# Performance work log

Hardware: AMD Instinct MI355X
Metric: run time of the kernel (lower is better)

Reference implementation:

```python
import jax, jax.numpy as jnp
import numpy as np

B, S, D, H = 8, 1024, 768, 12
DH = D // H


def setup_inputs() -> dict:
    key = jax.random.key(0)
    ks = jax.random.split(key, 6)
    scale = 1.0 / np.sqrt(D)
    return {
        "inputs": jax.random.normal(ks[0], (B, S, D), dtype=jnp.float32),
        "Wq": jax.random.normal(ks[1], (D, D), dtype=jnp.float32) * scale,
        "bq": jnp.zeros((D,), jnp.float32),
        "Wk": jax.random.normal(ks[2], (D, D), dtype=jnp.float32) * scale,
        "bk": jnp.zeros((D,), jnp.float32),
        "Wv": jax.random.normal(ks[3], (D, D), dtype=jnp.float32) * scale,
        "bv": jnp.zeros((D,), jnp.float32),
        "Wo": jax.random.normal(ks[4], (D, D), dtype=jnp.float32) * scale,
        "bo": jnp.zeros((D,), jnp.float32),
    }


def _split_heads(x):
    # [B,S,D] -> [B,H,S,DH]
    b, s, _ = x.shape
    return x.reshape(b, s, H, DH).transpose(0, 2, 1, 3)


def reference(inputs, Wq, bq, Wk, bk, Wv, bv, Wo, bo):
    q = _split_heads(inputs @ Wq + bq)
    k = _split_heads(inputs @ Wk + bk)
    v = _split_heads(inputs @ Wv + bv)
    # scaled dot-product attention; scale = sqrt(projection_dim)
    scores = jnp.einsum("bhqd,bhkd->bhqk", q, k) / jnp.sqrt(jnp.float32(DH))
    weights = jax.nn.softmax(scores, axis=-1)
    attn = jnp.einsum("bhqk,bhkd->bhqd", weights, v)
    attn = attn.transpose(0, 2, 1, 3).reshape(inputs.shape[0], -1, D)
    return attn @ Wo + bo
```

## Files before the change

kernel.cpp:

```cpp
#include <hip/hip_runtime.h>
#include <math.h>

#define B 8
#define S 1024
#define D 768
#define H 12
#define DH 64
#define M_TOT (B * S)

#define QSCALE 0.18033688011112042f

typedef short bf16x8 __attribute__((ext_vector_type(8)));
typedef float f32x4 __attribute__((ext_vector_type(4)));
typedef unsigned u32x4 __attribute__((ext_vector_type(4)));

__device__ __forceinline__ unsigned short f2bf(float x) {
    unsigned u = __builtin_bit_cast(unsigned, x);
    u = (u + 0x7FFFu + ((u >> 16) & 1u)) >> 16;
    return (unsigned short)u;
}
__device__ __forceinline__ unsigned short f2bf_ru(float x) {
    return (unsigned short)((__builtin_bit_cast(unsigned, x) + 0x8000u) >> 16);
}
__device__ __forceinline__ unsigned pk2bf_ru(float a, float b) {
    unsigned ua = __builtin_bit_cast(unsigned, a) + 0x8000u;
    unsigned ub = __builtin_bit_cast(unsigned, b) + 0x8000u;
    return __builtin_amdgcn_perm(ub, ua, 0x07060302u);
}

__device__ __forceinline__ void async16(const unsigned short* g, unsigned short* l) {
    __builtin_amdgcn_global_load_lds((const __attribute__((address_space(1))) void*)g,
                                     (__attribute__((address_space(3))) void*)l, 16, 0, 0);
}

__device__ __forceinline__ void stage_tiles(const unsigned short* __restrict__ A,
                                            const unsigned short* __restrict__ Bt,
                                            unsigned short* At, unsigned short* Bs,
                                            int m0, int n0, int k0, int w, int srow, int scol) {
#pragma unroll
    for (int c = 0; c < 2; ++c) {
        const int cc = w * 2 + c;
        const int row = cc * 16 + srow;
        async16(&A[(size_t)(m0 + row) * D + k0 + scol], &At[cc * 512]);
        async16(&Bt[(size_t)(n0 + row) * D + k0 + scol], &Bs[cc * 512]);
    }
}

__global__ __launch_bounds__(256) void prep(const float* __restrict__ inputs,
                                            unsigned short* __restrict__ Abf,
                                            const float* W0, const float* W1,
                                            const float* W2, const float* W3,
                                            unsigned short* T0, unsigned short* T1,
                                            unsigned short* T2, unsigned short* T3) {
    const int bid = blockIdx.x;
    const int t = threadIdx.x;
    if (bid < 6144) {
        const int i = (bid * 256 + t) * 4;
        const float4 v = *(const float4*)&inputs[i];
        ushort4 o;
        o.x = f2bf(v.x); o.y = f2bf(v.y); o.z = f2bf(v.z); o.w = f2bf(v.w);
        *(ushort4*)&Abf[i] = o;
    } else {
        const int id = bid - 6144;
        const int z = id / 144;
        const int rem = id % 144;
        const int kx = rem % 12, ny = rem / 12;
        const float* Wsrc[4] = {W0, W1, W2, W3};
        unsigned short* Tdst[4] = {T0, T1, T2, T3};
        const float* Wm = Wsrc[z];
        unsigned short* Tm = Tdst[z];
        __shared__ float tile[64][65];
        const int r = t >> 4, c4 = (t & 15) * 4;
        const int k0 = kx * 64, n0 = ny * 64;
#pragma unroll
        for (int rr = 0; rr < 4; ++rr) {
            const float4 v = *(const float4*)&Wm[(size_t)(k0 + r + rr * 16) * D + n0 + c4];
            tile[r + rr * 16][c4 + 0] = v.x;
            tile[r + rr * 16][c4 + 1] = v.y;
            tile[r + rr * 16][c4 + 2] = v.z;
            tile[r + rr * 16][c4 + 3] = v.w;
        }
        __syncthreads();
#pragma unroll
        for (int rr = 0; rr < 4; ++rr) {
            const int nr = r + rr * 16;
            ushort4 o;
            o.x = f2bf(tile[c4 + 0][nr]);
            o.y = f2bf(tile[c4 + 1][nr]);
            o.z = f2bf(tile[c4 + 2][nr]);
            o.w = f2bf(tile[c4 + 3][nr]);
            *(ushort4*)&Tm[(size_t)(n0 + nr) * D + k0 + c4] = o;
        }
    }
}

__global__ __launch_bounds__(256) void gemm_qkv(const unsigned short* __restrict__ A,
                                                const unsigned short* __restrict__ Wtq,
                                                const unsigned short* __restrict__ Wtk,
                                                const unsigned short* __restrict__ Wtv,
                                                const float* __restrict__ bq,
                                                const float* __restrict__ bk,
                                                const float* __restrict__ bv,
                                                unsigned short* __restrict__ Qb,
                                                unsigned short* __restrict__ Kb,
                                                unsigned short* __restrict__ Vtb) {
    __shared__ unsigned short At[3][128 * 32];
    __shared__ unsigned short Bs[3][128 * 32];
    const int z = blockIdx.z;
    const unsigned short* Bt = (z == 0) ? Wtq : (z == 1) ? Wtk : Wtv;
    const float* bias = (z == 0) ? bq : (z == 1) ? bk : bv;
    const float scale = (z == 0) ? QSCALE : 1.0f;

    const int t = threadIdx.x;
    const int w = t >> 6, lane = t & 63;
    const int quad = lane >> 4, l15 = lane & 15;
    const int m0 = blockIdx.x * 128, n0 = blockIdx.y * 128;
    const int wm = (w & 1) * 64, wn = (w >> 1) * 64;
    const int srow = lane >> 2, scol = (lane & 3) * 8;
    const int NT = D / 32;

    f32x4 acc[4][4];
#pragma unroll
    for (int i = 0; i < 4; ++i)
#pragma unroll
        for (int j = 0; j < 4; ++j) acc[i][j] = (f32x4){0.f, 0.f, 0.f, 0.f};

    stage_tiles(A, Bt, At[0], Bs[0], m0, n0, 0, w, srow, scol);
    stage_tiles(A, Bt, At[1], Bs[1], m0, n0, 32, w, srow, scol);
    int cur = 0, nxt = 2;
    for (int kt = 0; kt < NT; ++kt) {
        if (kt + 1 < NT) {
            __asm__ volatile("s_waitcnt vmcnt(4)" ::: "memory");
        } else {
            __asm__ volatile("s_waitcnt vmcnt(0)" ::: "memory");
        }
        __asm__ volatile("s_barrier" ::: "memory");
        if (kt + 2 < NT) {
            stage_tiles(A, Bt, At[nxt], Bs[nxt], m0, n0, (kt + 2) * 32, w, srow, scol);
            nxt = (nxt == 2) ? 0 : nxt + 1;
        }
        const unsigned short* Atc = At[cur];
        const unsigned short* Bsc = Bs[cur];
        cur = (cur == 2) ? 0 : cur + 1;
        bf16x8 af[4], bfr[4];
#pragma unroll
        for (int i = 0; i < 4; ++i)
            af[i] = *(const bf16x8*)&Atc[(wm + i * 16 + l15) * 32 + quad * 8];
#pragma unroll
        for (int j = 0; j < 4; ++j)
            bfr[j] = *(const bf16x8*)&Bsc[(wn + j * 16 + l15) * 32 + quad * 8];
#pragma unroll
        for (int i = 0; i < 4; ++i)
#pragma unroll
            for (int j = 0; j < 4; ++j)
                acc[i][j] = __builtin_amdgcn_mfma_f32_16x16x32_bf16(af[i], bfr[j], acc[i][j], 0, 0, 0);
    }

#pragma unroll
    for (int j = 0; j < 4; ++j) {
        const int col = n0 + wn + j * 16 + l15;
        const float bv2 = bias[col];
#pragma unroll
        for (int i = 0; i < 4; ++i) {
            const int row0 = m0 + wm + i * 16 + quad * 4;
            if (z < 2) {
                unsigned short* C = (z == 0) ? Qb : Kb;
#pragma unroll
                for (int r = 0; r < 4; ++r)
                    C[(size_t)(row0 + r) * D + col] = f2bf_ru((acc[i][j][r] + bv2) * scale);
            } else {
                const int h = col >> 6, dh = col & 63;
                const int bb = row0 >> 10, s0 = row0 & 1023;
                const int g = (s0 & 63) >> 2;
                const int kap = ((g >> 3) << 5) | ((g & 3) << 3) | (((g >> 2) & 1) << 2);
                const int s0p = (s0 & ~63) | kap;
                uint2 u;
                u.x = pk2bf_ru(acc[i][j][0] + bv2, acc[i][j][1] + bv2);
                u.y = pk2bf_ru(acc[i][j][2] + bv2, acc[i][j][3] + bv2);
                *(uint2*)&Vtb[((size_t)(bb * H + h) * DH + dh) * S + s0p] = u;
            }
        }
    }
}

__global__ __launch_bounds__(256) void gemm_out(const unsigned short* __restrict__ A,
                                                const unsigned short* __restrict__ Bt,
                                                const float* __restrict__ bias,
                                                float* __restrict__ C) {
    __shared__ unsigned short At[3][128 * 32];
    __shared__ unsigned short Bs[3][128 * 32];
    const int t = threadIdx.x;
    const int w = t >> 6, lane = t & 63;
    const int quad = lane >> 4, l15 = lane & 15;
    const int m0 = blockIdx.x * 128, n0 = blockIdx.y * 128;
    const int wm = (w & 1) * 64, wn = (w >> 1) * 64;
    const int srow = lane >> 2, scol = (lane & 3) * 8;
    const int NT = D / 32;

    f32x4 acc[4][4];
#pragma unroll
    for (int i = 0; i < 4; ++i)
#pragma unroll
        for (int j = 0; j < 4; ++j) acc[i][j] = (f32x4){0.f, 0.f, 0.f, 0.f};

    stage_tiles(A, Bt, At[0], Bs[0], m0, n0, 0, w, srow, scol);
    stage_tiles(A, Bt, At[1], Bs[1], m0, n0, 32, w, srow, scol);
    int cur = 0, nxt = 2;
    for (int kt = 0; kt < NT; ++kt) {
        if (kt + 1 < NT) {
            __asm__ volatile("s_waitcnt vmcnt(4)" ::: "memory");
        } else {
            __asm__ volatile("s_waitcnt vmcnt(0)" ::: "memory");
        }
        __asm__ volatile("s_barrier" ::: "memory");
        if (kt + 2 < NT) {
            stage_tiles(A, Bt, At[nxt], Bs[nxt], m0, n0, (kt + 2) * 32, w, srow, scol);
            nxt = (nxt == 2) ? 0 : nxt + 1;
        }
        const unsigned short* Atc = At[cur];
        const unsigned short* Bsc = Bs[cur];
        cur = (cur == 2) ? 0 : cur + 1;
        bf16x8 af[4], bfr[4];
#pragma unroll
        for (int i = 0; i < 4; ++i)
            af[i] = *(const bf16x8*)&Atc[(wm + i * 16 + l15) * 32 + quad * 8];
#pragma unroll
        for (int j = 0; j < 4; ++j)
            bfr[j] = *(const bf16x8*)&Bsc[(wn + j * 16 + l15) * 32 + quad * 8];
#pragma unroll
        for (int i = 0; i < 4; ++i)
#pragma unroll
            for (int j = 0; j < 4; ++j)
                acc[i][j] = __builtin_amdgcn_mfma_f32_16x16x32_bf16(af[i], bfr[j], acc[i][j], 0, 0, 0);
    }

#pragma unroll
    for (int j = 0; j < 4; ++j) {
        const int col = n0 + wn + j * 16 + l15;
        const float bv = bias[col];
#pragma unroll
        for (int i = 0; i < 4; ++i) {
            const int row0 = m0 + wm + i * 16 + quad * 4;
#pragma unroll
            for (int r = 0; r < 4; ++r) C[(size_t)(row0 + r) * D + col] = acc[i][j][r] + bv;
        }
    }
}

__global__ __launch_bounds__(256) void attn_mfma(const unsigned short* __restrict__ Qg,
                                                 const unsigned short* __restrict__ Kg,
                                                 const unsigned short* __restrict__ Vtg,
                                                 unsigned short* __restrict__ ATT) {
    __shared__ unsigned short Ks[3][2 * 64 * 32];
    __shared__ unsigned short Vs[3][2 * 64 * 32];

    const int t = threadIdx.x;
    const int w = t >> 6, lane = t & 63;
    const int quad = lane >> 4, l15 = lane & 15;
    const int bh = blockIdx.x % (B * H);
    const int q0 = (blockIdx.x / (B * H)) * 128;
    const int b = bh / H, h = bh % H;

    bf16x8 qb[2][2];
#pragma unroll
    for (int qh = 0; qh < 2; ++qh) {
        const size_t qoff = ((size_t)(b * S + q0 + w * 32 + qh * 16 + l15)) * D + h * DH;
        qb[qh][0] = *(const bf16x8*)&Qg[qoff + quad * 8];
        qb[qh][1] = *(const bf16x8*)&Qg[qoff + 32 + quad * 8];
    }

    f32x4 o[2][4];
#pragma unroll
    for (int qh = 0; qh < 2; ++qh)
#pragma unroll
        for (int n = 0; n < 4; ++n) o[qh][n] = (f32x4){0.f, 0.f, 0.f, 0.f};
    float l_acc[2] = {0.f, 0.f};

    const int srow = lane >> 2;
    const int scol = (((lane & 3) ^ ((lane >> 3) & 3))) * 8;
    const int fsw = ((quad ^ ((l15 >> 1) & 3)) * 8);
    const int NT = S / 64;

    #define STAGE(ktv, bf)                                                                   \
        {                                                                                     \
            const int _kt = (ktv);                                                            \
            _Pragma("unroll")                                                                 \
            for (int kc = 0; kc < 2; ++kc) {                                                  \
                async16(&Kg[((size_t)(b * S + _kt * 64 + w * 16 + srow)) * D + h * DH + kc * 32 + scol], \
                        &Ks[bf][kc * 2048 + w * 512]);                                        \
                async16(&Vtg[((size_t)(bh * DH + w * 16 + srow)) * S + _kt * 64 + kc * 32 + scol],       \
                        &Vs[bf][kc * 2048 + w * 512]);                                        \
            }                                                                                 \
        }

    STAGE(0, 0);
    STAGE(1, 1);
    int cur = 0, nxt = 2;
    for (int kt = 0; kt < NT; ++kt) {
        if (kt + 1 < NT) {
            __asm__ volatile("s_waitcnt vmcnt(4)" ::: "memory");
        } else {
            __asm__ volatile("s_waitcnt vmcnt(0)" ::: "memory");
        }
        __asm__ volatile("s_barrier" ::: "memory");
        if (kt + 2 < NT) {
            STAGE(kt + 2, nxt);
            nxt = (nxt == 2) ? 0 : nxt + 1;
        }
        const int buf = cur;
        cur = (cur == 2) ? 0 : cur + 1;

        f32x4 sc[2][4];
#pragma unroll
        for (int n = 0; n < 4; ++n) {
            const bf16x8 ka0 = *(const bf16x8*)&Ks[buf][0 * 2048 + (n * 16 + l15) * 32 + fsw];
            const bf16x8 ka1 = *(const bf16x8*)&Ks[buf][1 * 2048 + (n * 16 + l15) * 32 + fsw];
#pragma unroll
            for (int qh = 0; qh < 2; ++qh) {
                f32x4 zz = (f32x4){0.f, 0.f, 0.f, 0.f};
                zz = __builtin_amdgcn_mfma_f32_16x16x32_bf16(ka0, qb[qh][0], zz, 0, 0, 0);
                zz = __builtin_amdgcn_mfma_f32_16x16x32_bf16(ka1, qb[qh][1], zz, 0, 0, 0);
                sc[qh][n] = zz;
            }
        }

        bf16x8 pb[2][2];
#pragma unroll
        for (int qh = 0; qh < 2; ++qh) {
            float p[4][4];
            float rs = 0.f;
#pragma unroll
            for (int n = 0; n < 4; ++n) {
#pragma unroll
                for (int r = 0; r < 4; ++r) {
                    p[n][r] = __builtin_amdgcn_exp2f(sc[qh][n][r]);
                    rs += p[n][r];
                }
            }
            l_acc[qh] += rs;
            u32x4 u0, u1;
            u0.x = pk2bf_ru(p[0][0], p[0][1]);
            u0.y = pk2bf_ru(p[0][2], p[0][3]);
            u0.z = pk2bf_ru(p[1][0], p[1][1]);
            u0.w = pk2bf_ru(p[1][2], p[1][3]);
            u1.x = pk2bf_ru(p[2][0], p[2][1]);
            u1.y = pk2bf_ru(p[2][2], p[2][3]);
            u1.z = pk2bf_ru(p[3][0], p[3][1]);
            u1.w = pk2bf_ru(p[3][2], p[3][3]);
            pb[qh][0] = __builtin_bit_cast(bf16x8, u0);
            pb[qh][1] = __builtin_bit_cast(bf16x8, u1);
        }

#pragma unroll
        for (int n = 0; n < 4; ++n) {
            const bf16x8 va0 = *(const bf16x8*)&Vs[buf][0 * 2048 + (n * 16 + l15) * 32 + fsw];
            const bf16x8 va1 = *(const bf16x8*)&Vs[buf][1 * 2048 + (n * 16 + l15) * 32 + fsw];
#pragma unroll
            for (int qh = 0; qh < 2; ++qh) {
                o[qh][n] = __builtin_amdgcn_mfma_f32_16x16x32_bf16(va0, pb[qh][0], o[qh][n], 0, 0, 0);
                o[qh][n] = __builtin_amdgcn_mfma_f32_16x16x32_bf16(va1, pb[qh][1], o[qh][n], 0, 0, 0);
            }
        }
    }
    #undef STAGE

#pragma unroll
    for (int qh = 0; qh < 2; ++qh) {
        float l = l_acc[qh];
        l += __shfl_xor(l, 16, 64);
        l += __shfl_xor(l, 32, 64);
        const float inv = 1.0f / l;
        const size_t row = (size_t)(b * S + q0 + w * 32 + qh * 16 + l15) * D + h * DH;
#pragma unroll
        for (int n = 0; n < 4; ++n) {
            uint2 u;
            u.x = pk2bf_ru(o[qh][n][0] * inv, o[qh][n][1] * inv);
            u.y = pk2bf_ru(o[qh][n][2] * inv, o[qh][n][3] * inv);
            *(uint2*)&ATT[row + n * 16 + quad * 4] = u;
        }
    }
}

extern "C" void kernel_launch(void* const* d_in, const int* in_sizes, int n_in,
                              void* d_out, int out_size, void* d_ws, size_t ws_size,
                              hipStream_t stream) {
    const float* inputs = (const float*)d_in[0];
    const float* Wq = (const float*)d_in[1];
    const float* bq = (const float*)d_in[2];
    const float* Wk = (const float*)d_in[3];
    const float* bk = (const float*)d_in[4];
    const float* Wv = (const float*)d_in[5];
    const float* bv = (const float*)d_in[6];
    const float* Wo = (const float*)d_in[7];
    const float* bo = (const float*)d_in[8];

    const size_t nA = (size_t)M_TOT * D;
    unsigned short* Abf  = (unsigned short*)d_ws;
    unsigned short* Qb   = Abf + nA;
    unsigned short* Kb   = Qb + nA;
    unsigned short* Vtb  = Kb + nA;
    unsigned short* ATTb = Vtb + nA;
    unsigned short* Wtq  = ATTb + nA;
    unsigned short* Wtk  = Wtq + (size_t)D * D;
    unsigned short* Wtv  = Wtk + (size_t)D * D;
    unsigned short* Wto  = Wtv + (size_t)D * D;

    prep<<<6144 + 576, 256, 0, stream>>>(inputs, Abf, Wq, Wk, Wv, Wo, Wtq, Wtk, Wtv, Wto);

    gemm_qkv<<<dim3(M_TOT / 128, D / 128, 3), 256, 0, stream>>>(
        Abf, Wtq, Wtk, Wtv, bq, bk, bv, Qb, Kb, Vtb);

    attn_mfma<<<dim3((S / 128) * B * H), 256, 0, stream>>>(Qb, Kb, Vtb, ATTb);

    gemm_out<<<dim3(M_TOT / 128, D / 128), 256, 0, stream>>>(ATTb, Wto, bo, (float*)d_out);
}
```

Measured before the change: 199.1 us.

## Swizzle GEMM LDS tiles, swap MFMA operands for vectorized epilogue stores

Both projection GEMMs now write tiles into LDS with an XOR-swizzled column layout and read fragments back with the matching swizzle, which targets LDS bank conflicts on fragment reads. For the Q/K and output GEMMs the MFMA operands are swapped so each lane holds four consecutive output columns. That lets the epilogue do vectorized bias loads and packed bf16 or float4 stores instead of scalar strided stores. Global staging pointers are also precomputed in the GEMMs and the attention kernel to cut per-iteration address arithmetic. The cost is more index logic and a separate code path per projection type.

```diff
diff --git a/kernel.cpp b/kernel.cpp
--- a/kernel.cpp
+++ b/kernel.cpp
@@ -31,19 +31,6 @@
 __device__ __forceinline__ void async16(const unsigned short* g, unsigned short* l) {
     __builtin_amdgcn_global_load_lds((const __attribute__((address_space(1))) void*)g,
                                      (__attribute__((address_space(3))) void*)l, 16, 0, 0);
-}
-
-__device__ __forceinline__ void stage_tiles(const unsigned short* __restrict__ A,
-                                            const unsigned short* __restrict__ Bt,
-                                            unsigned short* At, unsigned short* Bs,
-                                            int m0, int n0, int k0, int w, int srow, int scol) {
-#pragma unroll
-    for (int c = 0; c < 2; ++c) {
-        const int cc = w * 2 + c;
-        const int row = cc * 16 + srow;
-        async16(&A[(size_t)(m0 + row) * D + k0 + scol], &At[cc * 512]);
-        async16(&Bt[(size_t)(n0 + row) * D + k0 + scol], &Bs[cc * 512]);
-    }
 }
 
 __global__ __launch_bounds__(256) void prep(const float* __restrict__ inputs,
@@ -116,17 +103,33 @@
     const int quad = lane >> 4, l15 = lane & 15;
     const int m0 = blockIdx.x * 128, n0 = blockIdx.y * 128;
     const int wm = (w & 1) * 64, wn = (w >> 1) * 64;
-    const int srow = lane >> 2, scol = (lane & 3) * 8;
+    const int srow = lane >> 2;
+    const int scolg = (((lane & 3) ^ ((lane >> 3) & 3))) * 8;
+    const int fsw = ((quad ^ ((l15 >> 1) & 3)) * 8);
     const int NT = D / 32;
 
+    const int r0 = (w * 2) * 16 + srow, r1 = r0 + 16;
+    const unsigned short* pa0 = &A[(size_t)(m0 + r0) * D + scolg];
+    const unsigned short* pa1 = &A[(size_t)(m0 + r1) * D + scolg];
+    const unsigned short* pb0 = &Bt[(size_t)(n0 + r0) * D + scolg];
+    const unsigned short* pb1 = &Bt[(size_t)(n0 + r1) * D + scolg];
+
+    #define GSTAGE(buf, k0)                                    \
+        {                                                      \
+            async16(pa0 + (k0), &At[buf][(w * 2) * 512]);      \
+            async16(pa1 + (k0), &At[buf][(w * 2 + 1) * 512]);  \
+            async16(pb0 + (k0), &Bs[buf][(w * 2) * 512]);      \
+            async16(pb1 + (k0), &Bs[buf][(w * 2 + 1) * 512]);  \
+        }
+
     f32x4 acc[4][4];
 #pragma unroll
     for (int i = 0; i < 4; ++i)
 #pragma unroll
         for (int j = 0; j < 4; ++j) acc[i][j] = (f32x4){0.f, 0.f, 0.f, 0.f};
 
-    stage_tiles(A, Bt, At[0], Bs[0], m0, n0, 0, w, srow, scol);
-    stage_tiles(A, Bt, At[1], Bs[1], m0, n0, 32, w, srow, scol);
+    GSTAGE(0, 0);
+    GSTAGE(1, 32);
     int cur = 0, nxt = 2;
     for (int kt = 0; kt < NT; ++kt) {
         if (kt + 1 < NT) {
@@ -136,7 +139,7 @@
         }
         __asm__ volatile("s_barrier" ::: "memory");
         if (kt + 2 < NT) {
-            stage_tiles(A, Bt, At[nxt], Bs[nxt], m0, n0, (kt + 2) * 32, w, srow, scol);
+            GSTAGE(nxt, (kt + 2) * 32);
             nxt = (nxt == 2) ? 0 : nxt + 1;
         }
         const unsigned short* Atc = At[cur];
@@ -145,30 +148,49 @@
         bf16x8 af[4], bfr[4];
 #pragma unroll
         for (int i = 0; i < 4; ++i)
-            af[i] = *(const bf16x8*)&Atc[(wm + i * 16 + l15) * 32 + quad * 8];
+            af[i] = *(const bf16x8*)&Atc[(wm + i * 16 + l15) * 32 + fsw];
 #pragma unroll
         for (int j = 0; j < 4; ++j)
-            bfr[j] = *(const bf16x8*)&Bsc[(wn + j * 16 + l15) * 32 + quad * 8];
-#pragma unroll
-        for (int i = 0; i < 4; ++i)
-#pragma unroll
-            for (int j = 0; j < 4; ++j)
-                acc[i][j] = __builtin_amdgcn_mfma_f32_16x16x32_bf16(af[i], bfr[j], acc[i][j], 0, 0, 0);
-    }
-
-#pragma unroll
-    for (int j = 0; j < 4; ++j) {
-        const int col = n0 + wn + j * 16 + l15;
-        const float bv2 = bias[col];
-#pragma unroll
-        for (int i = 0; i < 4; ++i) {
-            const int row0 = m0 + wm + i * 16 + quad * 4;
-            if (z < 2) {
-                unsigned short* C = (z == 0) ? Qb : Kb;
-#pragma unroll
-                for (int r = 0; r < 4; ++r)
-                    C[(size_t)(row0 + r) * D + col] = f2bf_ru((acc[i][j][r] + bv2) * scale);
-            } else {
+            bfr[j] = *(const bf16x8*)&Bsc[(wn + j * 16 + l15) * 32 + fsw];
+        if (z < 2) {
+#pragma unroll
+            for (int i = 0; i < 4; ++i)
+#pragma unroll
+                for (int j = 0; j < 4; ++j)
+                    acc[i][j] = __builtin_amdgcn_mfma_f32_16x16x32_bf16(bfr[j], af[i], acc[i][j], 0, 0, 0);
+        } else {
+#pragma unroll
+            for (int i = 0; i < 4; ++i)
+#pragma unroll
+                for (int j = 0; j < 4; ++j)
+                    acc[i][j] = __builtin_amdgcn_mfma_f32_16x16x32_bf16(af[i], bfr[j], acc[i][j], 0, 0, 0);
+        }
+    }
+    #undef GSTAGE
+
+    if (z < 2) {
+        unsigned short* C = (z == 0) ? Qb : Kb;
+#pragma unroll
+        for (int j = 0; j < 4; ++j) {
+            const int nb = n0 + wn + j * 16 + quad * 4;
+            const float4 bb = *(const float4*)&bias[nb];
+#pragma unroll
+            for (int i = 0; i < 4; ++i) {
+                const int m = m0 + wm + i * 16 + l15;
+                uint2 u;
+                u.x = pk2bf_ru((acc[i][j][0] + bb.x) * scale, (acc[i][j][1] + bb.y) * scale);
+                u.y = pk2bf_ru((acc[i][j][2] + bb.z) * scale, (acc[i][j][3] + bb.w) * scale);
+                *(uint2*)&C[(size_t)m * D + nb] = u;
+            }
+        }
+    } else {
+#pragma unroll
+        for (int j = 0; j < 4; ++j) {
+            const int col = n0 + wn + j * 16 + l15;
+            const float bv2 = bias[col];
+#pragma unroll
+            for (int i = 0; i < 4; ++i) {
+                const int row0 = m0 + wm + i * 16 + quad * 4;
                 const int h = col >> 6, dh = col & 63;
                 const int bb = row0 >> 10, s0 = row0 & 1023;
                 const int g = (s0 & 63) >> 2;
@@ -194,17 +216,33 @@
     const int quad = lane >> 4, l15 = lane & 15;
     const int m0 = blockIdx.x * 128, n0 = blockIdx.y * 128;
     const int wm = (w & 1) * 64, wn = (w >> 1) * 64;
-    const int srow = lane >> 2, scol = (lane & 3) * 8;
+    const int srow = lane >> 2;
+    const int scolg = (((lane & 3) ^ ((lane >> 3) & 3))) * 8;
+    const int fsw = ((quad ^ ((l15 >> 1) & 3)) * 8);
     const int NT = D / 32;
 
+    const int r0 = (w * 2) * 16 + srow, r1 = r0 + 16;
+    const unsigned short* pa0 = &A[(size_t)(m0 + r0) * D + scolg];
+    const unsigned short* pa1 = &A[(size_t)(m0 + r1) * D + scolg];
+    const unsigned short* pb0 = &Bt[(size_t)(n0 + r0) * D + scolg];
+    const unsigned short* pb1 = &Bt[(size_t)(n0 + r1) * D + scolg];
+
+    #define GSTAGE(buf, k0)                                    \
+        {                                                      \
+            async16(pa0 + (k0), &At[buf][(w * 2) * 512]);      \
+            async16(pa1 + (k0), &At[buf][(w * 2 + 1) * 512]);  \
+            async16(pb0 + (k0), &Bs[buf][(w * 2) * 512]);      \
+            async16(pb1 + (k0), &Bs[buf][(w * 2 + 1) * 512]);  \
+        }
+
     f32x4 acc[4][4];
 #pragma unroll
     for (int i = 0; i < 4; ++i)
 #pragma unroll
         for (int j = 0; j < 4; ++j) acc[i][j] = (f32x4){0.f, 0.f, 0.f, 0.f};
 
-    stage_tiles(A, Bt, At[0], Bs[0], m0, n0, 0, w, srow, scol);
-    stage_tiles(A, Bt, At[1], Bs[1], m0, n0, 32, w, srow, scol);
+    GSTAGE(0, 0);
+    GSTAGE(1, 32);
     int cur = 0, nxt = 2;
     for (int kt = 0; kt < NT; ++kt) {
         if (kt + 1 < NT) {
@@ -214,7 +252,7 @@
         }
         __asm__ volatile("s_barrier" ::: "memory");
         if (kt + 2 < NT) {
-            stage_tiles(A, Bt, At[nxt], Bs[nxt], m0, n0, (kt + 2) * 32, w, srow, scol);
+            GSTAGE(nxt, (kt + 2) * 32);
             nxt = (nxt == 2) ? 0 : nxt + 1;
         }
         const unsigned short* Atc = At[cur];
@@ -223,26 +261,31 @@
         bf16x8 af[4], bfr[4];
 #pragma unroll
         for (int i = 0; i < 4; ++i)
-            af[i] = *(const bf16x8*)&Atc[(wm + i * 16 + l15) * 32 + quad * 8];
+            af[i] = *(const bf16x8*)&Atc[(wm + i * 16 + l15) * 32 + fsw];
 #pragma unroll
         for (int j = 0; j < 4; ++j)
-            bfr[j] = *(const bf16x8*)&Bsc[(wn + j * 16 + l15) * 32 + quad * 8];
+            bfr[j] = *(const bf16x8*)&Bsc[(wn + j * 16 + l15) * 32 + fsw];
 #pragma unroll
         for (int i = 0; i < 4; ++i)
 #pragma unroll
             for (int j = 0; j < 4; ++j)
-                acc[i][j] = __builtin_amdgcn_mfma_f32_16x16x32_bf16(af[i], bfr[j], acc[i][j], 0, 0, 0);
-    }
+                acc[i][j] = __builtin_amdgcn_mfma_f32_16x16x32_bf16(bfr[j], af[i], acc[i][j], 0, 0, 0);
+    }
+    #undef GSTAGE
 
 #pragma unroll
     for (int j = 0; j < 4; ++j) {
-        const int col = n0 + wn + j * 16 + l15;
-        const float bv = bias[col];
+        const int nb = n0 + wn + j * 16 + quad * 4;
+        const float4 bb = *(const float4*)&bias[nb];
 #pragma unroll
         for (int i = 0; i < 4; ++i) {
-            const int row0 = m0 + wm + i * 16 + quad * 4;
-#pragma unroll
-            for (int r = 0; r < 4; ++r) C[(size_t)(row0 + r) * D + col] = acc[i][j][r] + bv;
+            const int m = m0 + wm + i * 16 + l15;
+            float4 o;
+            o.x = acc[i][j][0] + bb.x;
+            o.y = acc[i][j][1] + bb.y;
+            o.z = acc[i][j][2] + bb.z;
+            o.w = acc[i][j][3] + bb.w;
+            *(float4*)&C[(size_t)m * D + nb] = o;
         }
     }
 }
@@ -281,16 +324,18 @@
     const int fsw = ((quad ^ ((l15 >> 1) & 3)) * 8);
     const int NT = S / 64;
 
-    #define STAGE(ktv, bf)                                                                   \
-        {                                                                                     \
-            const int _kt = (ktv);                                                            \
-            _Pragma("unroll")                                                                 \
-            for (int kc = 0; kc < 2; ++kc) {                                                  \
-                async16(&Kg[((size_t)(b * S + _kt * 64 + w * 16 + srow)) * D + h * DH + kc * 32 + scol], \
-                        &Ks[bf][kc * 2048 + w * 512]);                                        \
-                async16(&Vtg[((size_t)(bh * DH + w * 16 + srow)) * S + _kt * 64 + kc * 32 + scol],       \
-                        &Vs[bf][kc * 2048 + w * 512]);                                        \
-            }                                                                                 \
+    const unsigned short* kbase = Kg + ((size_t)(b * S + w * 16 + srow)) * D + h * DH + scol;
+    const unsigned short* vbase = Vtg + ((size_t)(bh * DH + w * 16 + srow)) * S + scol;
+
+    #define STAGE(ktv, bf)                                                       \
+        {                                                                        \
+            _Pragma("unroll")                                                    \
+            for (int kc = 0; kc < 2; ++kc) {                                     \
+                async16(kbase + (size_t)(ktv) * 64 * D + kc * 32,                \
+                        &Ks[bf][kc * 2048 + w * 512]);                           \
+                async16(vbase + (ktv) * 64 + kc * 32,                            \
+                        &Vs[bf][kc * 2048 + w * 512]);                           \
+            }                                                                    \
         }
 
     STAGE(0, 0);
```

Measured after the change: 216.3 us. +8.6%, slower.
